# Kernel tuning notes

Hardware: AMD Instinct MI355X
Metric: run time of the kernel (lower is better)

The kernel has to match this reference:

```python
import jax, jax.numpy as jnp
import numpy as np

N_NODES = 100000
N_EDGES = 1600000
N_GRAPHS = 512
IN_CH = 64
HID = 128
LAT = 64
MAX_NODES = 128
OUT_SIZE = MAX_NODES * (MAX_NODES - 1) // 2  # 8128


def _gcn_conv(x, W, b, src, dst, n):
    """PyG GCNConv: x' = D^-1/2 (A+I) D^-1/2 (x W) + b, degrees include self-loops."""
    h = x @ W  # [N, out]
    deg = jnp.zeros((n,), h.dtype).at[dst].add(1.0) + 1.0  # in-degree + self-loop
    dinv = jax.lax.rsqrt(deg)
    norm = dinv[src] * dinv[dst]  # [E]
    agg = jnp.zeros_like(h).at[dst].add(h[src] * norm[:, None])  # neighbor scatter-add
    agg = agg + h * (dinv * dinv)[:, None]  # self-loop term, norm = 1/deg
    return agg + b


def setup_inputs() -> dict:
    key = jax.random.key(0)
    ks = jax.random.split(key, 20)
    s = 0.02
    inp = {
        "x": jax.random.normal(ks[0], (N_NODES, IN_CH), jnp.float32),
        "edge_index": jax.random.randint(ks[1], (2, N_EDGES), 0, N_NODES),
        "batch": jnp.sort(jax.random.randint(ks[2], (N_NODES,), 0, N_GRAPHS)),
        "eps": jax.random.normal(ks[3], (N_GRAPHS, LAT), jnp.float32),
        # encoder params
        "W1": jax.random.normal(ks[4], (IN_CH, HID), jnp.float32) * s,
        "b1": jnp.zeros((HID,), jnp.float32),
        "W2": jax.random.normal(ks[5], (HID, HID), jnp.float32) * s,
        "b2": jnp.zeros((HID,), jnp.float32),
        "Wmu": jax.random.normal(ks[6], (HID, LAT), jnp.float32) * s,
        "bmu": jnp.zeros((LAT,), jnp.float32),
        "Wlv": jax.random.normal(ks[7], (HID, LAT), jnp.float32) * s,
        "blv": jnp.zeros((LAT,), jnp.float32),
        # decoder MLP params
        "D1": jax.random.normal(ks[8], (LAT, HID), jnp.float32) * s,
        "d1": jnp.zeros((HID,), jnp.float32),
        "D2": jax.random.normal(ks[9], (HID, HID), jnp.float32) * s,
        "d2": jnp.zeros((HID,), jnp.float32),
        "D3": jax.random.normal(ks[10], (HID, OUT_SIZE), jnp.float32) * s,
        "d3": jnp.zeros((OUT_SIZE,), jnp.float32),
    }
    return inp


def reference(x, edge_index, batch, eps, W1, b1, W2, b2, Wmu, bmu, Wlv, blv,
              D1, d1, D2, d2, D3, d3):
    src, dst = edge_index[0], edge_index[1]
    # --- encoder: two GCN layers + ReLU ---
    h = jax.nn.relu(_gcn_conv(x, W1, b1, src, dst, N_NODES))
    h = jax.nn.relu(_gcn_conv(h, W2, b2, src, dst, N_NODES))
    # --- global mean pool by graph id ---
    sums = jax.ops.segment_sum(h, batch, num_segments=N_GRAPHS)
    cnts = jax.ops.segment_sum(jnp.ones((N_NODES,), h.dtype), batch, num_segments=N_GRAPHS)
    h_graph = sums / jnp.maximum(cnts, 1.0)[:, None]  # [G, HID]
    mu = h_graph @ Wmu + bmu
    logvar = h_graph @ Wlv + blv
    # --- reparameterise ---
    z = mu + eps * jnp.exp(0.5 * logvar)  # [G, LAT]
    # --- MLP decoder -> symmetric adjacency ---
    p = jax.nn.relu(z @ D1 + d1)
    p = jax.nn.relu(p @ D2 + d2)
    probs = jax.nn.sigmoid(p @ D3 + d3)  # [G, OUT_SIZE]
    r, c = jnp.triu_indices(MAX_NODES, k=1)
    adj = jnp.zeros((N_GRAPHS, MAX_NODES, MAX_NODES), probs.dtype)
    adj = adj.at[:, r, c].set(probs)
    adj = adj + jnp.swapaxes(adj, 1, 2)
    return adj, mu, logvar
```

## Files before the change

### kernel.cpp

```cpp
#include <hip/hip_runtime.h>
#include <hip/hip_fp16.h>

#define NN 100000
#define NE 1600000
#define NG 512
#define OUTS 8128
#define NB2 196
#define CHUNK 8192
#define NPB 196

typedef short bf16x8 __attribute__((ext_vector_type(8)));
typedef _Float16 f16x8 __attribute__((ext_vector_type(8)));
typedef _Float16 f16x2 __attribute__((ext_vector_type(2)));
typedef float f32x4 __attribute__((ext_vector_type(4)));

__device__ __forceinline__ unsigned pack_bf16x2(float a, float b) {
    unsigned ua = __float_as_uint(a);
    unsigned ub = __float_as_uint(b);
    ua = (ua + 0x7fffu + ((ua >> 16) & 1u)) >> 16;
    ub = (ub + 0x7fffu + ((ub >> 16) & 1u)) >> 16;
    return ua | (ub << 16);
}
__device__ __forceinline__ unsigned short f2bf(float f) {
    unsigned u = __float_as_uint(f);
    u = (u + 0x7fffu + ((u >> 16) & 1u)) >> 16;
    return (unsigned short)u;
}
__device__ __forceinline__ unsigned cvt_pkrtz_u(float a, float b) {
    auto h = __builtin_amdgcn_cvt_pkrtz(a, b);
    union { decltype(h) h2; unsigned u; } c; c.h2 = h; return c.u;
}
__device__ __forceinline__ f16x2 u2h(unsigned u) { union { unsigned u; f16x2 h; } c; c.u = u; return c.h; }

__device__ __forceinline__ unsigned f2fp8(float f) {
    unsigned h = (unsigned)__half_as_ushort(__float2half(f * 0.00390625f));
    return (h + 0x3Fu + ((h >> 7) & 1u)) >> 7;
}

__global__ __launch_bounds__(512) void k_part(const int* __restrict__ src, const int* __restrict__ dst,
        int* __restrict__ tmp, int* __restrict__ scanhist) {
    __shared__ int hist[NB2], cur[NB2], scan[256];
    int p = blockIdx.x, t = threadIdx.x;
    int e0 = p * CHUNK;
    int e1 = min(e0 + CHUNK, NE);
    for (int i = t; i < NB2; i += 512) hist[i] = 0;
    __syncthreads();
    for (int e = e0 + t; e < e1; e += 512)
        atomicAdd(&hist[dst[e] >> 9], 1);
    __syncthreads();
    int h = 0;
    if (t < 256) { h = (t < NB2) ? hist[t] : 0; scan[t] = h; }
    __syncthreads();
    for (int off = 1; off < 256; off <<= 1) {
        int v = (t < 256 && t >= off) ? scan[t - off] : 0;
        __syncthreads();
        if (t < 256) scan[t] += v;
        __syncthreads();
    }
    if (t < NB2) {
        int excl = scan[t] - h;
        cur[t] = excl;
        scanhist[p * (NB2 + 1) + t] = excl;
    }
    if (t == 0) scanhist[p * (NB2 + 1) + NB2] = e1 - e0;
    __syncthreads();
    for (int e = e0 + t; e < e1; e += 512) {
        int d = dst[e];
        int b = d >> 9;
        int r = atomicAdd(&cur[b], 1);
        tmp[e0 + r] = (src[e] << 9) | (d & 511);
    }
}

__global__ __launch_bounds__(256) void k_btotseg(const int* __restrict__ scanhist,
        int* __restrict__ bucketbase, const int* __restrict__ batch, int* __restrict__ seg_end) {
    if (blockIdx.x == 0) {
        __shared__ int sc[256];
        int b = threadIdx.x;
        int tot = 0;
        if (b < NB2) {
            for (int p = 0; p < NPB; ++p)
                tot += scanhist[p * (NB2 + 1) + b + 1] - scanhist[p * (NB2 + 1) + b];
        }
        sc[b] = tot;
        __syncthreads();
        for (int off = 1; off < 256; off <<= 1) {
            int v = (b >= off) ? sc[b - off] : 0;
            __syncthreads();
            sc[b] += v;
            __syncthreads();
        }
        if (b < NB2) bucketbase[b] = sc[b] - tot;
    } else {
        int i = (blockIdx.x - 1) * 256 + threadIdx.x;
        if (i >= NN) return;
        int b = batch[i];
        int bn = (i == NN - 1) ? NG : batch[i + 1];
        for (int g = b; g < bn; ++g) seg_end[g] = i + 1;
        if (i == 0) {
            for (int g = 0; g < b; ++g) seg_end[g] = 0;
        }
    }
}

__global__ __launch_bounds__(1024) void k_fill2(const int* __restrict__ bucketbase,
        const int* __restrict__ scanhist, const int* __restrict__ tmp,
        int* __restrict__ colidx, int* __restrict__ cnti, int* __restrict__ rowptr,
        float* __restrict__ dinv) {
    __shared__ int lc[512], rb[512], sc[256];
    int b = blockIdx.x, t = threadIdx.x;
    int n0 = b << 9;
    if (t < 512) lc[t] = 0;
    __syncthreads();
    int w = t >> 6, lane = t & 63;
    for (int p = w; p < NPB; p += 16) {
        int s0 = scanhist[p * (NB2 + 1) + b];
        int s1 = scanhist[p * (NB2 + 1) + b + 1];
        int base = p * CHUNK;
        for (int i = s0 + lane; i < s1; i += 64)
            atomicAdd(&lc[tmp[base + i] & 511], 1);
    }
    __syncthreads();
    int v0 = 0, v1 = 0, s = 0;
    if (t < 256) { v0 = lc[2 * t]; v1 = lc[2 * t + 1]; s = v0 + v1; sc[t] = s; }
    __syncthreads();
    for (int off = 1; off < 256; off <<= 1) {
        int x = (t < 256 && t >= off) ? sc[t - off] : 0;
        __syncthreads();
        if (t < 256) sc[t] += x;
        __syncthreads();
    }
    if (t < 256) {
        int excl = sc[t] - s;
        int base0 = bucketbase[b];
        rb[2 * t] = base0 + excl;
        rb[2 * t + 1] = base0 + excl + v0;
        int node0 = n0 + 2 * t;
        if (node0 < NN) {
            cnti[node0] = v0;
            rowptr[node0] = base0 + excl;
            dinv[node0] = rsqrtf((float)v0 + 1.0f);
        }
        if (node0 + 1 < NN) {
            cnti[node0 + 1] = v1;
            rowptr[node0 + 1] = base0 + excl + v0;
            dinv[node0 + 1] = rsqrtf((float)v1 + 1.0f);
        }
    }
    __syncthreads();
    if (t < 512) lc[t] = 0;
    __syncthreads();
    for (int p = w; p < NPB; p += 16) {
        int s0 = scanhist[p * (NB2 + 1) + b];
        int s1 = scanhist[p * (NB2 + 1) + b + 1];
        int base = p * CHUNK;
        for (int i = s0 + lane; i < s1; i += 64) {
            int v = tmp[base + i];
            int dl = v & 511;
            int pos = atomicAdd(&lc[dl], 1);
            colidx[rb[dl] + pos] = v >> 9;
        }
    }
}

__global__ __launch_bounds__(256) void k_wtall(const float* __restrict__ W1,
        const float* __restrict__ W2, const float* __restrict__ D3,
        unsigned short* __restrict__ wt1, unsigned short* __restrict__ wt2,
        unsigned short* __restrict__ wt3) {
    int i = blockIdx.x * 256 + threadIdx.x;
    if (i < 8192) {
        int n = i >> 6, k = i & 63;
        wt1[i] = (unsigned short)__half_as_ushort(__float2half(W1[k * 128 + n]));
    } else if (i < 24576) {
        int e = i - 8192;
        int n = e >> 7, k = e & 127;
        wt2[e] = f2bf(W2[k * 128 + n]);
    } else {
        int e = i - 24576;
        if (e < 128 * OUTS) wt3[e] = f2bf(D3[e]);
    }
}

__global__ __launch_bounds__(256) void k_scale_x(const float* __restrict__ x,
        const float* __restrict__ dinv, unsigned* __restrict__ u1) {
    int i = blockIdx.x * 256 + threadIdx.x;
    int row = i >> 5, c = i & 31;
    float2 v = *(const float2*)&x[(long)row * 64 + c * 2];
    float d = dinv[row];
    u1[i] = cvt_pkrtz_u(v.x * d, v.y * d);
}

__global__ __launch_bounds__(256) void k_gather1(const int* __restrict__ rowptr,
        const int* __restrict__ cnti, const int* __restrict__ colidx,
        const unsigned* __restrict__ u, const float* __restrict__ dinv,
        unsigned* __restrict__ s1) {
    int node = blockIdx.x * 32 + (threadIdx.x >> 3);
    int lane = threadIdx.x & 7;
    const uint4* uf = (const uint4*)u;
    uint4 self = uf[node * 8 + lane];
    f16x2 a0 = u2h(self.x), a1 = u2h(self.y), a2 = u2h(self.z), a3 = u2h(self.w);
    f16x2 z = {(_Float16)0.f, (_Float16)0.f};
    f16x2 b0 = z, b1 = z, b2 = z, b3 = z;
    int n = cnti[node];
    const int* ci = colidx + rowptr[node];
    int j = 0;
    for (; j + 4 <= n; j += 4) {
        uint4 va = uf[ci[j] * 8 + lane];
        uint4 vb = uf[ci[j + 1] * 8 + lane];
        uint4 vc = uf[ci[j + 2] * 8 + lane];
        uint4 vd = uf[ci[j + 3] * 8 + lane];
        a0 += u2h(va.x); a1 += u2h(va.y); a2 += u2h(va.z); a3 += u2h(va.w);
        b0 += u2h(vb.x); b1 += u2h(vb.y); b2 += u2h(vb.z); b3 += u2h(vb.w);
        a0 += u2h(vc.x); a1 += u2h(vc.y); a2 += u2h(vc.z); a3 += u2h(vc.w);
        b0 += u2h(vd.x); b1 += u2h(vd.y); b2 += u2h(vd.z); b3 += u2h(vd.w);
    }
    for (; j < n; ++j) {
        uint4 va = uf[ci[j] * 8 + lane];
        a0 += u2h(va.x); a1 += u2h(va.y); a2 += u2h(va.z); a3 += u2h(va.w);
    }
    a0 += b0; a1 += b1; a2 += b2; a3 += b3;
    float d = dinv[node];
    uint4 o;
    o.x = cvt_pkrtz_u((float)a0[0] * d, (float)a0[1] * d);
    o.y = cvt_pkrtz_u((float)a1[0] * d, (float)a1[1] * d);
    o.z = cvt_pkrtz_u((float)a2[0] * d, (float)a2[1] * d);
    o.w = cvt_pkrtz_u((float)a3[0] * d, (float)a3[1] * d);
    *(uint4*)&s1[node * 32 + lane * 4] = o;
}

#define DECO(W, LO, HI) { LO += u2h(((W) & 0x007f007fu) << 7); HI += u2h(((W) & 0x7f007f00u) >> 1); }
__global__ __launch_bounds__(256) void k_gather2(const int* __restrict__ rowptr,
        const int* __restrict__ cnti, const int* __restrict__ colidx,
        const unsigned* __restrict__ u, const float* __restrict__ dinv,
        unsigned* __restrict__ s2) {
    int node = blockIdx.x * 32 + (threadIdx.x >> 3);
    int lane = threadIdx.x & 7;
    const uint4* uf = (const uint4*)u;
    uint4 self = uf[node * 8 + lane];
    f16x2 z = {(_Float16)0.f, (_Float16)0.f};
    f16x2 la0 = z, ha0 = z, la1 = z, ha1 = z, la2 = z, ha2 = z, la3 = z, ha3 = z;
    f16x2 lb0 = z, hb0 = z, lb1 = z, hb1 = z, lb2 = z, hb2 = z, lb3 = z, hb3 = z;
    DECO(self.x, la0, ha0) DECO(self.y, la1, ha1) DECO(self.z, la2, ha2) DECO(self.w, la3, ha3)
    int n = cnti[node];
    const int* ci = colidx + rowptr[node];
    int j = 0;
    for (; j + 4 <= n; j += 4) {
        uint4 va = uf[ci[j] * 8 + lane];
        uint4 vb = uf[ci[j + 1] * 8 + lane];
        uint4 vc = uf[ci[j + 2] * 8 + lane];
        uint4 vd = uf[ci[j + 3] * 8 + lane];
        DECO(va.x, la0, ha0) DECO(va.y, la1, ha1) DECO(va.z, la2, ha2) DECO(va.w, la3, ha3)
        DECO(vb.x, lb0, hb0) DECO(vb.y, lb1, hb1) DECO(vb.z, lb2, hb2) DECO(vb.w, lb3, hb3)
        DECO(vc.x, la0, ha0) DECO(vc.y, la1, ha1) DECO(vc.z, la2, ha2) DECO(vc.w, la3, ha3)
        DECO(vd.x, lb0, hb0) DECO(vd.y, lb1, hb1) DECO(vd.z, lb2, hb2) DECO(vd.w, lb3, hb3)
    }
    for (; j < n; ++j) {
        uint4 va = uf[ci[j] * 8 + lane];
        DECO(va.x, la0, ha0) DECO(va.y, la1, ha1) DECO(va.z, la2, ha2) DECO(va.w, la3, ha3)
    }
    la0 += lb0; ha0 += hb0; la1 += lb1; ha1 += hb1;
    la2 += lb2; ha2 += hb2; la3 += lb3; ha3 += hb3;
    float d = dinv[node] * 16.0f;
    uint4 o1, o2;
    o1.x = pack_bf16x2((float)la0[0] * d, (float)ha0[0] * d);
    o1.y = pack_bf16x2((float)la0[1] * d, (float)ha0[1] * d);
    o1.z = pack_bf16x2((float)la1[0] * d, (float)ha1[0] * d);
    o1.w = pack_bf16x2((float)la1[1] * d, (float)ha1[1] * d);
    o2.x = pack_bf16x2((float)la2[0] * d, (float)ha2[0] * d);
    o2.y = pack_bf16x2((float)la2[1] * d, (float)ha2[1] * d);
    o2.z = pack_bf16x2((float)la3[0] * d, (float)ha3[0] * d);
    o2.w = pack_bf16x2((float)la3[1] * d, (float)ha3[1] * d);
    *(uint4*)&s2[node * 64 + lane * 8] = o1;
    *(uint4*)&s2[node * 64 + lane * 8 + 4] = o2;
}

template<int K, int EPI, int AF16>
__global__ __launch_bounds__(256) void k_gemm_mfma(const unsigned short* __restrict__ Ab,
        const unsigned short* __restrict__ wt, const float* __restrict__ dinv,
        const float* __restrict__ bias, void* __restrict__ outp) {
    constexpr int KS = K / 32;
    constexpr int SLOTS = K / 8;
    __shared__ __align__(16) unsigned short wlds[128 * K];
    char* lb = (char*)wlds;
    for (int c = threadIdx.x; c < 128 * SLOTS; c += 256) {
        int n = c / SLOTS, s = c - n * SLOTS;
        *(uint4*)(lb + n * (2 * K) + ((s ^ (n & 7)) << 4)) = *(const uint4*)(wt + c * 8);
    }
    __syncthreads();
    int lane = threadIdx.x & 63;
    int w = threadIdx.x >> 6;
    int r0 = blockIdx.x * 64 + w * 16;
    int arow = r0 + (lane & 15);
    if (arow >= NN) arow = NN - 1;
    bf16x8 af[KS];
    #pragma unroll
    for (int ks = 0; ks < KS; ++ks)
        af[ks] = *(const bf16x8*)&Ab[(long)arow * K + ks * 32 + (lane >> 4) * 8];
    f32x4 acc[8];
    #pragma unroll
    for (int t = 0; t < 8; ++t) acc[t] = (f32x4){0.f, 0.f, 0.f, 0.f};
    #pragma unroll
    for (int ks = 0; ks < KS; ++ks) {
        #pragma unroll
        for (int t = 0; t < 8; ++t) {
            int n = t * 16 + (lane & 15);
            int slot = ks * 4 + (lane >> 4);
            bf16x8 braw = *(const bf16x8*)(lb + n * (2 * K) + ((slot ^ (n & 7)) << 4));
            if constexpr (AF16) {
                union { bf16x8 r; f16x8 h; } ca, cb;
                ca.r = af[ks]; cb.r = braw;
                acc[t] = __builtin_amdgcn_mfma_f32_16x16x32_f16(ca.h, cb.h, acc[t], 0, 0, 0);
            } else {
                acc[t] = __builtin_amdgcn_mfma_f32_16x16x32_bf16(af[ks], braw, acc[t], 0, 0, 0);
            }
        }
    }
    float bv[8];
    #pragma unroll
    for (int t = 0; t < 8; ++t) bv[t] = bias[t * 16 + (lane & 15)];
    #pragma unroll
    for (int r = 0; r < 4; ++r) {
        long row = r0 + (lane >> 4) * 4 + r;
        if (row >= NN) continue;
        float d = dinv[row];
        #pragma unroll
        for (int t = 0; t < 8; ++t) {
            float val = fmaxf(acc[t][r] + bv[t], 0.f);
            int col = t * 16 + (lane & 15);
            if (EPI == 0)
                ((unsigned char*)outp)[row * 128 + col] = (unsigned char)f2fp8(val * (16.0f * d));
            else
                ((unsigned short*)outp)[row * 128 + col] = f2bf(val);
        }
    }
}

__global__ __launch_bounds__(256) void k_poolmean(const unsigned* __restrict__ h,
        const int* __restrict__ seg_end, float* __restrict__ hg) {
    __shared__ float part[3][128];
    int g = blockIdx.x;
    int w = threadIdx.x >> 6, t = threadIdx.x & 63;
    int s = (g == 0) ? 0 : seg_end[g - 1];
    int e = seg_end[g];
    float a0 = 0.f, a1 = 0.f;
    for (int i = s + w; i < e; i += 4) {
        unsigned u = h[(long)i * 64 + t];
        a0 += __uint_as_float(u << 16);
        a1 += __uint_as_float(u & 0xffff0000u);
    }
    if (w) { part[w - 1][t * 2] = a0; part[w - 1][t * 2 + 1] = a1; }
    __syncthreads();
    if (w == 0) {
        a0 += part[0][t * 2] + part[1][t * 2] + part[2][t * 2];
        a1 += part[0][t * 2 + 1] + part[1][t * 2 + 1] + part[2][t * 2 + 1];
        float inv = (e > s) ? 1.0f / (float)(e - s) : 0.f;
        float2 o = { a0 * inv, a1 * inv };
        *(float2*)&hg[g * 128 + t * 2] = o;
    }
}

__global__ __launch_bounds__(128) void k_decfused(const float* __restrict__ hg,
        const float* __restrict__ Wmu, const float* __restrict__ bmu,
        const float* __restrict__ Wlv, const float* __restrict__ blv,
        const float* __restrict__ eps,
        const float* __restrict__ D1, const float* __restrict__ d1,
        const float* __restrict__ D2, const float* __restrict__ d2,
        float* __restrict__ mu_o, float* __restrict__ lv_o, float* __restrict__ p2out) {
    __shared__ float row[128], mlv[128], zr[64], p1[128];
    int g = blockIdx.x, t = threadIdx.x;
    row[t] = hg[g * 128 + t];
    __syncthreads();
    if (t < 64) {
        float acc = bmu[t];
        for (int k = 0; k < 128; ++k) acc += row[k] * Wmu[k * 64 + t];
        mlv[t] = acc;
    } else {
        int t2 = t - 64;
        float acc = blv[t2];
        for (int k = 0; k < 128; ++k) acc += row[k] * Wlv[k * 64 + t2];
        mlv[64 + t2] = acc;
    }
    __syncthreads();
    if (t < 64) {
        float mu = mlv[t], lv = mlv[64 + t];
        mu_o[g * 64 + t] = mu;
        lv_o[g * 64 + t] = lv;
        zr[t] = mu + eps[g * 64 + t] * expf(0.5f * lv);
    }
    __syncthreads();
    float acc = d1[t];
    for (int k = 0; k < 64; ++k) acc += zr[k] * D1[k * 128 + t];
    p1[t] = fmaxf(acc, 0.f);
    __syncthreads();
    acc = d2[t];
    for (int k = 0; k < 128; ++k) acc += p1[k] * D2[k * 128 + t];
    p2out[g * 128 + t] = fmaxf(acc, 0.f);
}

__global__ __launch_bounds__(256) void k_dec3(const float* __restrict__ A,
        const unsigned short* __restrict__ Wb, const float* __restrict__ b, float* __restrict__ out) {
    __shared__ float alds[16][128];
    int m0 = blockIdx.y * 16;
    for (int i = threadIdx.x; i < 16 * 128; i += 256)
        alds[i >> 7][i & 127] = A[(m0 + (i >> 7)) * 128 + (i & 127)];
    __syncthreads();
    if (threadIdx.x >= 254) return;
    int c = blockIdx.x * 1016 + threadIdx.x * 4;
    float4 bb = *(const float4*)&b[c];
    float4 acc[16];
    #pragma unroll
    for (int r = 0; r < 16; ++r) acc[r] = bb;
    for (int k = 0; k < 128; ++k) {
        uint2 u = *(const uint2*)&Wb[(long)k * OUTS + c];
        float w0 = __uint_as_float(u.x << 16);
        float w1 = __uint_as_float(u.x & 0xffff0000u);
        float w2 = __uint_as_float(u.y << 16);
        float w3 = __uint_as_float(u.y & 0xffff0000u);
        #pragma unroll
        for (int r = 0; r < 16; ++r) {
            float a = alds[r][k];
            acc[r].x += a * w0; acc[r].y += a * w1;
            acc[r].z += a * w2; acc[r].w += a * w3;
        }
    }
    #pragma unroll
    for (int r = 0; r < 16; ++r) {
        float4 o;
        o.x = 1.f / (1.f + expf(-acc[r].x));
        o.y = 1.f / (1.f + expf(-acc[r].y));
        o.z = 1.f / (1.f + expf(-acc[r].z));
        o.w = 1.f / (1.f + expf(-acc[r].w));
        *(float4*)&out[(long)(m0 + r) * OUTS + c] = o;
    }
}

__global__ __launch_bounds__(256) void k_adj(const float* __restrict__ probs, float* __restrict__ adj) {
    int t = blockIdx.x * 256 + threadIdx.x;
    int g = t >> 12;
    int rem = t & 4095;
    int r = rem >> 5;
    int c0 = (rem & 31) * 4;
    const float* pg = &probs[g * OUTS];
    float4 o;
    float* op = (float*)&o;
    #pragma unroll
    for (int j = 0; j < 4; ++j) {
        int c = c0 + j;
        if (c == r) { op[j] = 0.f; continue; }
        int a = c < r ? c : r;
        int b = c < r ? r : c;
        int k = a * (255 - a) / 2 + (b - a - 1);
        op[j] = pg[k];
    }
    *(float4*)&adj[(long)t * 4] = o;
}

extern "C" void kernel_launch(void* const* d_in, const int* in_sizes, int n_in,
                              void* d_out, int out_size, void* d_ws, size_t ws_size,
                              hipStream_t stream) {
    const float* x   = (const float*)d_in[0];
    const int*   ei  = (const int*)d_in[1];
    const int* batch = (const int*)d_in[2];
    const float* eps = (const float*)d_in[3];
    const float* W1  = (const float*)d_in[4];
    const float* b1  = (const float*)d_in[5];
    const float* W2  = (const float*)d_in[6];
    const float* b2  = (const float*)d_in[7];
    const float* Wmu = (const float*)d_in[8];
    const float* bmu = (const float*)d_in[9];
    const float* Wlv = (const float*)d_in[10];
    const float* blv = (const float*)d_in[11];
    const float* D1  = (const float*)d_in[12];
    const float* d1  = (const float*)d_in[13];
    const float* D2  = (const float*)d_in[14];
    const float* d2  = (const float*)d_in[15];
    const float* D3  = (const float*)d_in[16];
    const float* d3  = (const float*)d_in[17];

    const int* esrc = ei;
    const int* edst = ei + NE;

    float* out  = (float*)d_out;
    float* mu_o = out + 8388608;
    float* lv_o = mu_o + 32768;

    int*   colidx   = (int*)out;
    int*   cnti     = colidx + 1600000;
    int*   rowptr   = cnti + 100000;
    int*   seg_end  = rowptr + 100000;
    float* dinv     = (float*)(seg_end + 512);
    int*   scanhist = (int*)(dinv + 100000);
    int*   bucketbase = scanhist + 38612;
    unsigned short* wt3 = (unsigned short*)(bucketbase + 256);

    float* ws = (float*)d_ws;
    unsigned* u1u = (unsigned*)ws;
    unsigned* s1u = u1u + 3200000;
    unsigned char* u2b = (unsigned char*)(ws + 6400000);
    unsigned* s2u = (unsigned*)(ws + 9600000);
    unsigned* h2b = (unsigned*)(ws + 16000000);
    unsigned short* wt1 = (unsigned short*)(ws + 22400000);
    unsigned short* wt2 = wt1 + 8192;
    int* tmp = (int*)(ws + 22420000);
    float* hg    = ws;
    float* p2    = hg + 65536;
    float* probs = p2 + 65536;

    k_part<<<NPB, 512, 0, stream>>>(esrc, edst, tmp, scanhist);
    k_btotseg<<<392, 256, 0, stream>>>(scanhist, bucketbase, batch, seg_end);
    k_fill2<<<NB2, 1024, 0, stream>>>(bucketbase, scanhist, tmp, colidx, cnti, rowptr, dinv);

    k_wtall<<<4161, 256, 0, stream>>>(W1, W2, D3, wt1, wt2, wt3);

    k_scale_x<<<12500, 256, 0, stream>>>(x, dinv, u1u);
    k_gather1<<<3125, 256, 0, stream>>>(rowptr, cnti, colidx, u1u, dinv, s1u);
    k_gemm_mfma<64, 0, 1><<<1563, 256, 0, stream>>>((const unsigned short*)s1u, wt1, dinv, b1, u2b);

    k_gather2<<<3125, 256, 0, stream>>>(rowptr, cnti, colidx, (const unsigned*)u2b, dinv, s2u);
    k_gemm_mfma<128, 1, 0><<<1563, 256, 0, stream>>>((const unsigned short*)s2u, wt2, dinv, b2, h2b);

    k_poolmean<<<NG, 256, 0, stream>>>(h2b, seg_end, hg);
    k_decfused<<<NG, 128, 0, stream>>>(hg, Wmu, bmu, Wlv, blv, eps, D1, d1, D2, d2,
                                       mu_o, lv_o, p2);

    dim3 g3(8, 32);
    k_dec3<<<g3, 256, 0, stream>>>(p2, wt3, d3, probs);
    k_adj<<<8192, 256, 0, stream>>>(probs, out);
}
```

Baseline: 240.6 us.

## Run decoder output GEMM on MFMA with fp16 operands and transposed weights

Replaces the scalar FMA decoder output layer with an MFMA 16x16x32 fp16 kernel. D3 is converted to fp16 and transposed through a shared-memory tile kernel so each lane reads contiguous K-slices. The p2 activations are also stored as fp16. This is meant to cut the ALU cost of the 512x128x8128 GEMM, at the cost of fp16 precision and output stores that are less coalesced (scattered per-element).

```diff
diff --git a/kernel.cpp b/kernel.cpp
--- a/kernel.cpp
+++ b/kernel.cpp
@@ -164,9 +164,8 @@
 }
 
 __global__ __launch_bounds__(256) void k_wtall(const float* __restrict__ W1,
-        const float* __restrict__ W2, const float* __restrict__ D3,
-        unsigned short* __restrict__ wt1, unsigned short* __restrict__ wt2,
-        unsigned short* __restrict__ wt3) {
+        const float* __restrict__ W2,
+        unsigned short* __restrict__ wt1, unsigned short* __restrict__ wt2) {
     int i = blockIdx.x * 256 + threadIdx.x;
     if (i < 8192) {
         int n = i >> 6, k = i & 63;
@@ -175,9 +174,22 @@
         int e = i - 8192;
         int n = e >> 7, k = e & 127;
         wt2[e] = f2bf(W2[k * 128 + n]);
-    } else {
-        int e = i - 24576;
-        if (e < 128 * OUTS) wt3[e] = f2bf(D3[e]);
+    }
+}
+
+__global__ __launch_bounds__(256) void k_wt3t(const float* __restrict__ D3,
+        unsigned short* __restrict__ o) {
+    __shared__ float tile[32][33];
+    int n0 = blockIdx.x * 32, k0 = blockIdx.y * 32;
+    for (int i = threadIdx.x; i < 1024; i += 256) {
+        int kk = i >> 5, nn = i & 31;
+        tile[kk][nn] = D3[(long)(k0 + kk) * OUTS + n0 + nn];
+    }
+    __syncthreads();
+    for (int i = threadIdx.x; i < 1024; i += 256) {
+        int nn = i >> 5, kk = i & 31;
+        o[(long)(n0 + nn) * 128 + k0 + kk] =
+            (unsigned short)__half_as_ushort(__float2half(tile[kk][nn]));
     }
 }
 
@@ -365,7 +377,8 @@
         const float* __restrict__ eps,
         const float* __restrict__ D1, const float* __restrict__ d1,
         const float* __restrict__ D2, const float* __restrict__ d2,
-        float* __restrict__ mu_o, float* __restrict__ lv_o, float* __restrict__ p2out) {
+        float* __restrict__ mu_o, float* __restrict__ lv_o,
+        unsigned short* __restrict__ p2out) {
     __shared__ float row[128], mlv[128], zr[64], p1[128];
     int g = blockIdx.x, t = threadIdx.x;
     row[t] = hg[g * 128 + t];
@@ -394,43 +407,47 @@
     __syncthreads();
     acc = d2[t];
     for (int k = 0; k < 128; ++k) acc += p1[k] * D2[k * 128 + t];
-    p2out[g * 128 + t] = fmaxf(acc, 0.f);
-}
-
-__global__ __launch_bounds__(256) void k_dec3(const float* __restrict__ A,
-        const unsigned short* __restrict__ Wb, const float* __restrict__ b, float* __restrict__ out) {
-    __shared__ float alds[16][128];
-    int m0 = blockIdx.y * 16;
-    for (int i = threadIdx.x; i < 16 * 128; i += 256)
-        alds[i >> 7][i & 127] = A[(m0 + (i >> 7)) * 128 + (i & 127)];
-    __syncthreads();
-    if (threadIdx.x >= 254) return;
-    int c = blockIdx.x * 1016 + threadIdx.x * 4;
-    float4 bb = *(const float4*)&b[c];
-    float4 acc[16];
-    #pragma unroll
-    for (int r = 0; r < 16; ++r) acc[r] = bb;
-    for (int k = 0; k < 128; ++k) {
-        uint2 u = *(const uint2*)&Wb[(long)k * OUTS + c];
-        float w0 = __uint_as_float(u.x << 16);
-        float w1 = __uint_as_float(u.x & 0xffff0000u);
-        float w2 = __uint_as_float(u.y << 16);
-        float w3 = __uint_as_float(u.y & 0xffff0000u);
+    p2out[g * 128 + t] = (unsigned short)__half_as_ushort(__float2half(fmaxf(acc, 0.f)));
+}
+
+__global__ __launch_bounds__(256) void k_dec3m(const unsigned short* __restrict__ Ab,
+        const unsigned short* __restrict__ Wt, const float* __restrict__ b,
+        float* __restrict__ out) {
+    int lane = threadIdx.x & 63;
+    int w = threadIdx.x >> 6;
+    int r0 = blockIdx.x * 64 + w * 16;
+    int c0 = blockIdx.y * 64;
+    int arow = r0 + (lane & 15);
+    f16x8 af[4];
+    #pragma unroll
+    for (int ks = 0; ks < 4; ++ks) {
+        union { bf16x8 r; f16x8 h; } ca;
+        ca.r = *(const bf16x8*)&Ab[arow * 128 + ks * 32 + (lane >> 4) * 8];
+        af[ks] = ca.h;
+    }
+    f32x4 acc[4];
+    #pragma unroll
+    for (int nt = 0; nt < 4; ++nt) acc[nt] = (f32x4){0.f, 0.f, 0.f, 0.f};
+    #pragma unroll
+    for (int nt = 0; nt < 4; ++nt) {
+        long n = c0 + nt * 16 + (lane & 15);
         #pragma unroll
-        for (int r = 0; r < 16; ++r) {
-            float a = alds[r][k];
-            acc[r].x += a * w0; acc[r].y += a * w1;
-            acc[r].z += a * w2; acc[r].w += a * w3;
-        }
-    }
-    #pragma unroll
-    for (int r = 0; r < 16; ++r) {
-        float4 o;
-        o.x = 1.f / (1.f + expf(-acc[r].x));
-        o.y = 1.f / (1.f + expf(-acc[r].y));
-        o.z = 1.f / (1.f + expf(-acc[r].z));
-        o.w = 1.f / (1.f + expf(-acc[r].w));
-        *(float4*)&out[(long)(m0 + r) * OUTS + c] = o;
+        for (int ks = 0; ks < 4; ++ks) {
+            union { bf16x8 r; f16x8 h; } cb;
+            cb.r = *(const bf16x8*)&Wt[n * 128 + ks * 32 + (lane >> 4) * 8];
+            acc[nt] = __builtin_amdgcn_mfma_f32_16x16x32_f16(af[ks], cb.h, acc[nt], 0, 0, 0);
+        }
+    }
+    #pragma unroll
+    for (int nt = 0; nt < 4; ++nt) {
+        int col = c0 + nt * 16 + (lane & 15);
+        float bias = b[col];
+        #pragma unroll
+        for (int r = 0; r < 4; ++r) {
+            int row = r0 + (lane >> 4) * 4 + r;
+            float v = acc[nt][r] + bias;
+            out[(long)row * OUTS + col] = 1.f / (1.f + expf(-v));
+        }
     }
 }
 
@@ -491,7 +508,7 @@
     float* dinv     = (float*)(seg_end + 512);
     int*   scanhist = (int*)(dinv + 100000);
     int*   bucketbase = scanhist + 38612;
-    unsigned short* wt3 = (unsigned short*)(bucketbase + 256);
+    unsigned short* wt3t = (unsigned short*)(bucketbase + 256);
 
     float* ws = (float*)d_ws;
     unsigned* u1u = (unsigned*)ws;
@@ -502,15 +519,17 @@
     unsigned short* wt1 = (unsigned short*)(ws + 22400000);
     unsigned short* wt2 = wt1 + 8192;
     int* tmp = (int*)(ws + 22420000);
-    float* hg    = ws;
-    float* p2    = hg + 65536;
-    float* probs = p2 + 65536;
+    float* hg = ws;
+    unsigned short* p2b = (unsigned short*)(hg + 65536);
+    float* probs = hg + 131072;
 
     k_part<<<NPB, 512, 0, stream>>>(esrc, edst, tmp, scanhist);
     k_btotseg<<<392, 256, 0, stream>>>(scanhist, bucketbase, batch, seg_end);
     k_fill2<<<NB2, 1024, 0, stream>>>(bucketbase, scanhist, tmp, colidx, cnti, rowptr, dinv);
 
-    k_wtall<<<4161, 256, 0, stream>>>(W1, W2, D3, wt1, wt2, wt3);
+    k_wtall<<<96, 256, 0, stream>>>(W1, W2, wt1, wt2);
+    dim3 gt(254, 4);
+    k_wt3t<<<gt, 256, 0, stream>>>(D3, wt3t);
 
     k_scale_x<<<12500, 256, 0, stream>>>(x, dinv, u1u);
     k_gather1<<<3125, 256, 0, stream>>>(rowptr, cnti, colidx, u1u, dinv, s1u);
@@ -521,9 +540,9 @@
 
     k_poolmean<<<NG, 256, 0, stream>>>(h2b, seg_end, hg);
     k_decfused<<<NG, 128, 0, stream>>>(hg, Wmu, bmu, Wlv, blv, eps, D1, d1, D2, d2,
-                                       mu_o, lv_o, p2);
-
-    dim3 g3(8, 32);
-    k_dec3<<<g3, 256, 0, stream>>>(p2, wt3, d3, probs);
+                                       mu_o, lv_o, p2b);
+
+    dim3 g3(8, 127);
+    k_dec3m<<<g3, 256, 0, stream>>>(p2b, wt3t, d3, probs);
     k_adj<<<8192, 256, 0, stream>>>(probs, out);
 }
```

Result: faster. 220.6 us (-8.3%).
